# Optimization experiments

Measured on AMD Instinct MI355X. Metric: run time of the kernel, lower is better.

## Reference

```python
import jax, jax.numpy as jnp
import numpy as np

B, D_IMG, D_TXT, E = 4096, 768, 768, 512
LAMBDA_CMP = 1.0
EPS = 1e-10


def setup_inputs() -> dict:
    key = jax.random.key(0)
    k1, k2, k3, k4, k5 = jax.random.split(key, 5)
    return {
        "images": jax.random.normal(k1, (B, D_IMG), dtype=jnp.float32),
        "texts": jax.random.normal(k2, (B, D_TXT), dtype=jnp.float32),
        "labels": jax.random.randint(k3, (B,), 0, 1000, dtype=jnp.int32),
        "W_img": jax.random.normal(k4, (D_IMG, E), dtype=jnp.float32) / np.sqrt(D_IMG),
        "W_txt": jax.random.normal(k5, (D_TXT, E), dtype=jnp.float32) / np.sqrt(D_TXT),
        "logit_scale": jnp.asarray(np.log(1.0 / 0.07), dtype=jnp.float32),
    }


def reference(images, texts, labels, W_img, W_txt, logit_scale):
    # CLIP-style encoders: linear project + L2 normalize
    img = images @ W_img
    txt = texts @ W_txt
    img = img / jnp.linalg.norm(img, axis=-1, keepdims=True)
    txt = txt / jnp.linalg.norm(txt, axis=-1, keepdims=True)
    logits = jnp.exp(logit_scale) * (img @ txt.T)  # [B, B]

    b = logits.shape[0]
    rows = jnp.arange(b)
    logp = jax.nn.log_softmax(logits, axis=-1)
    clip_loss = -jnp.mean(logp[rows, labels])

    probs = jnp.exp(logp)                # softmax probs [B, B]
    p_yi = probs[rows, labels]           # [B]
    # columns j whose label differs from sample i's label AND prob exceeds p_yi
    diff_label = labels[None, :] != labels[:, None]           # [B, B]
    mask = diff_label & (probs > p_yi[:, None])               # [B, B]
    denom = jnp.sum(jnp.where(mask, probs, 0.0), axis=1)      # [B]
    has_any = jnp.any(mask, axis=1)
    cmp_loss = jnp.sum(jnp.where(has_any, p_yi / (denom + EPS), 0.0)) / b

    return clip_loss + LAMBDA_CMP * cmp_loss
```

## Files before the change

### kernel.cpp

```cpp
#include <hip/hip_runtime.h>
#include <stdint.h>

#define BATCH 4096
#define DDIM  768
#define EDIM  512
#define NSPLIT 16
#define LOG2E 1.44269504088896340736f

using short8  = __attribute__((ext_vector_type(8))) short;
using float4v = __attribute__((ext_vector_type(4))) float;

__device__ __forceinline__ unsigned short f2bf(float x) {
    union { float f; uint32_t u; } v; v.f = x;
    uint32_t u = v.u;
    u += 0x7FFFu + ((u >> 16) & 1u);
    return (unsigned short)(u >> 16);
}
__device__ __forceinline__ float bf2f(unsigned short h) {
    union { uint32_t u; float f; } v; v.u = ((uint32_t)h) << 16;
    return v.f;
}

__device__ __forceinline__ short8 cvt8(float4 v0, float4 v1) {
    union { short8 s8; uint32_t w[4]; } u;
    asm("v_cvt_pk_bf16_f32 %0, %1, %2" : "=v"(u.w[0]) : "v"(v0.x), "v"(v0.y));
    asm("v_cvt_pk_bf16_f32 %0, %1, %2" : "=v"(u.w[1]) : "v"(v0.z), "v"(v0.w));
    asm("v_cvt_pk_bf16_f32 %0, %1, %2" : "=v"(u.w[2]) : "v"(v1.x), "v"(v1.y));
    asm("v_cvt_pk_bf16_f32 %0, %1, %2" : "=v"(u.w[3]) : "v"(v1.z), "v"(v1.w));
    return u.s8;
}

__device__ __forceinline__ void gl2lds16(const void* g, void* l) {
    __builtin_amdgcn_global_load_lds(
        (const __attribute__((address_space(1))) void*)g,
        (__attribute__((address_space(3))) void*)l, 16, 0, 0);
}

__global__ void transpose2(const float* __restrict__ Wa, const float* __restrict__ Wb,
                           unsigned short* __restrict__ Ta, unsigned short* __restrict__ Tb) {
    const float* W = blockIdx.z ? Wb : Wa;
    unsigned short* Wt = blockIdx.z ? Tb : Ta;
    __shared__ float tile[32][33];
    int n0 = blockIdx.x * 32, k0 = blockIdx.y * 32;
    int tid = threadIdx.x;
    for (int p = 0; p < 4; ++p) {
        int e = tid + p * 256; int lr = e >> 5, lc = e & 31;
        tile[lc][lr] = W[(size_t)(k0 + lr) * EDIM + n0 + lc];
    }
    __syncthreads();
    for (int p = 0; p < 4; ++p) {
        int e = tid + p * 256; int lr = e >> 5, lc = e & 31;
        Wt[(size_t)(n0 + lr) * DDIM + k0 + lc] = f2bf(tile[lr][lc]);
    }
}

__global__ __launch_bounds__(256) void gemm_nt(const float* __restrict__ Aimg,
                                               const float* __restrict__ Atxt,
                                               const unsigned short* __restrict__ Bimg,
                                               const unsigned short* __restrict__ Btxt,
                                               unsigned short* __restrict__ Cimg,
                                               unsigned short* __restrict__ Ctxt) {
    const float* A           = blockIdx.z ? Atxt : Aimg;
    const unsigned short* Bm = blockIdx.z ? Btxt : Bimg;
    unsigned short* C        = blockIdx.z ? Ctxt : Cimg;
    __shared__ __align__(16) float As[2][128 * 64];
    __shared__ __align__(16) unsigned short Bs[2][64 * 64];
    int tid = threadIdx.x;
    int wave = tid >> 6, lane = tid & 63;
    int q = lane >> 4, r = lane & 15;
    int m0 = blockIdx.x * 128, n0 = blockIdx.y * 64;
    int sw = (r >> 1) & 3;

    const float* gsA[8];
    float* lsA[8];
    for (int i = 0; i < 8; ++i) {
        int p = i * 256 + tid;
        int row = p >> 4, kqp = p & 15;
        int kq = kqp ^ (row & 7);
        gsA[i] = &A[(size_t)(m0 + row) * DDIM + kq * 4];
        lsA[i] = &As[0][p * 4];
    }
    const unsigned short* gsB[2];
    unsigned short* lsB[2];
    for (int i = 0; i < 2; ++i) {
        int u = i * 256 + tid;
        int kc2 = u >> 8, row = (u >> 2) & 63, kq = u & 3;
        int kq2 = kq ^ ((row >> 1) & 3);
        gsB[i] = &Bm[(size_t)(n0 + row) * DDIM + kc2 * 32 + kq2 * 8];
        lsB[i] = &Bs[0][u * 8];
    }

    float4v acc[2][4];
    for (int a = 0; a < 2; ++a)
        for (int t = 0; t < 4; ++t) acc[a][t] = (float4v){0.f, 0.f, 0.f, 0.f};

    for (int i = 0; i < 8; ++i) gl2lds16(gsA[i], lsA[i]);
    for (int i = 0; i < 2; ++i) gl2lds16(gsB[i], lsB[i]);
    __syncthreads();

    for (int it = 0; it < DDIM / 64; ++it) {
        int b = it & 1;
        if (it < DDIM / 64 - 1) {
            int k0 = (it + 1) * 64;
            for (int i = 0; i < 8; ++i) gl2lds16(gsA[i] + k0, lsA[i] + (b ^ 1) * (128 * 64));
            for (int i = 0; i < 2; ++i) gl2lds16(gsB[i] + k0, lsB[i] + (b ^ 1) * (64 * 64));
        }
        #pragma unroll
        for (int kc2 = 0; kc2 < 2; ++kc2) {
            int R0r = wave * 32 + r;
            int g0 = kc2 * 8 + (q ^ sw) * 2;
            int e = R0r & 7;
            int p0 = g0 ^ e, p1 = (g0 + 1) ^ e;
            float4 v0 = *(const float4*)&As[b][R0r * 64 + p0 * 4];
            float4 v1 = *(const float4*)&As[b][R0r * 64 + p1 * 4];
            float4 w0 = *(const float4*)&As[b][(R0r + 16) * 64 + p0 * 4];
            float4 w1 = *(const float4*)&As[b][(R0r + 16) * 64 + p1 * 4];
            short8 a0 = cvt8(v0, v1);
            short8 a1 = cvt8(w0, w1);
            #pragma unroll
            for (int t = 0; t < 4; ++t) {
                short8 bfr = *(const short8*)&Bs[b][kc2 * 2048 + (t * 16 + r) * 32 + (q ^ sw) * 8];
                acc[0][t] = __builtin_amdgcn_mfma_f32_16x16x32_bf16(a0, bfr, acc[0][t], 0, 0, 0);
                acc[1][t] = __builtin_amdgcn_mfma_f32_16x16x32_bf16(a1, bfr, acc[1][t], 0, 0, 0);
            }
        }
        __syncthreads();
    }
    for (int rg = 0; rg < 2; ++rg)
        for (int t = 0; t < 4; ++t)
            for (int g = 0; g < 4; ++g)
                C[(size_t)(m0 + wave * 32 + rg * 16 + q * 4 + g) * EDIM + n0 + t * 16 + r] =
                    f2bf(acc[rg][t][g]);
}

__global__ void rnorm(const unsigned short* __restrict__ pi, const unsigned short* __restrict__ pt,
                      const int* __restrict__ labels,
                      float* __restrict__ rn_i, float* __restrict__ rn_t,
                      float* __restrict__ tout) {
    int wave = threadIdx.x >> 6, lane = threadIdx.x & 63;
    int row = blockIdx.x * 4 + wave;
    int lab = labels[row];
    union { unsigned short us[8]; uint4 u4; } a, b, c;
    a.u4 = *(const uint4*)&pi[(size_t)row * 512 + lane * 8];
    b.u4 = *(const uint4*)&pt[(size_t)row * 512 + lane * 8];
    c.u4 = *(const uint4*)&pt[(size_t)lab * 512 + lane * 8];
    float si = 0.f, st = 0.f, sl = 0.f, dt = 0.f;
    #pragma unroll
    for (int j = 0; j < 8; ++j) {
        float fa = bf2f(a.us[j]), fb = bf2f(b.us[j]), fc = bf2f(c.us[j]);
        si += fa * fa; st += fb * fb; sl += fc * fc; dt += fa * fc;
    }
    for (int off = 1; off < 64; off <<= 1) {
        si += __shfl_xor(si, off);
        st += __shfl_xor(st, off);
        sl += __shfl_xor(sl, off);
        dt += __shfl_xor(dt, off);
    }
    if (lane == 0) {
        float ri = rsqrtf(si);
        rn_i[row] = ri;
        rn_t[row] = rsqrtf(st);
        tout[row] = dt * ri * rsqrtf(sl);
    }
}

__global__ __launch_bounds__(256) void flash_pass(
    const unsigned short* __restrict__ img, const unsigned short* __restrict__ txt,
    const int* __restrict__ labels, const float* __restrict__ tvals,
    const float* __restrict__ rn_i, const float* __restrict__ rn_t,
    const float* __restrict__ ls,
    float* __restrict__ lP, float* __restrict__ dP) {
    __shared__ __align__(16) unsigned short Bs[8 * 64 * 32];
    int tid = threadIdx.x;
    int wave = tid >> 6, lane = tid & 63;
    int q = lane >> 4, r = lane & 15;
    int row0 = blockIdx.x * 64 + wave * 16;
    int split = blockIdx.y;
    float alpha = expf(ls[0]);
    float c1 = alpha * LOG2E;

    int srow = tid >> 2, skp = tid & 3;
    int skp2 = skp ^ ((srow >> 1) & 3);
    int sw = (r >> 1) & 3;

    short8 af[16];
    for (int kc = 0; kc < 16; ++kc)
        af[kc] = *(const short8*)&img[(size_t)(row0 + r) * 512 + kc * 32 + q * 8];

    int labr[4]; float tr[4], rnr[4];
    for (int g = 0; g < 4; ++g) {
        int rw = row0 + q * 4 + g;
        labr[g] = labels[rw];
        tr[g] = tvals[rw];
        rnr[g] = rn_i[rw];
    }
    float l[4] = {0.f, 0.f, 0.f, 0.f}, d[4] = {0.f, 0.f, 0.f, 0.f};

    for (int ct = 0; ct < 4; ++ct) {
        int colbase = split * 256 + ct * 64;
        const unsigned short* gB = &txt[(size_t)(colbase + srow) * 512 + skp2 * 8];
        float4v acc[4];
        for (int t = 0; t < 4; ++t) acc[t] = (float4v){0.f, 0.f, 0.f, 0.f};
        for (int h = 0; h < 2; ++h) {
            __syncthreads();
            for (int i = 0; i < 8; ++i)
                gl2lds16(gB + h * 256 + i * 32, &Bs[i * 2048 + tid * 8]);
            __syncthreads();
            for (int kc = 0; kc < 8; ++kc) {
                short8 a = af[h * 8 + kc];
                for (int t = 0; t < 4; ++t) {
                    short8 bf = *(const short8*)&Bs[(kc * 64 + t * 16 + r) * 32 + (q ^ sw) * 8];
                    acc[t] = __builtin_amdgcn_mfma_f32_16x16x32_bf16(a, bf, acc[t], 0, 0, 0);
                }
            }
        }
        for (int t = 0; t < 4; ++t) {
            int cix = colbase + t * 16 + r;
            int lc = labels[cix];
            float rc = rn_t[cix];
            for (int g = 0; g < 4; ++g) {
                float a = acc[t][g] * (rc * rnr[g]);
                float p = exp2f(fmaf(a, c1, -c1));
                l[g] += p;
                d[g] += ((a > tr[g]) && (lc != labr[g])) ? p : 0.f;
            }
        }
    }
    for (int g = 0; g < 4; ++g) {
        float lv = l[g], dv = d[g];
        for (int off = 1; off < 16; off <<= 1) {
            lv += __shfl_xor(lv, off);
            dv += __shfl_xor(dv, off);
        }
        if (r == 0) {
            int rw = row0 + q * 4 + g;
            lP[(size_t)rw * NSPLIT + split] = lv;
            dP[(size_t)rw * NSPLIT + split] = dv;
        }
    }
}

__global__ void combine(const float* __restrict__ lP, const float* __restrict__ dP,
                        const float* __restrict__ tvals, const float* __restrict__ ls,
                        float* __restrict__ out) {
    int row = blockIdx.x * 256 + threadIdx.x;
    float alpha = expf(ls[0]);
    float L = 0.f, D = 0.f;
    for (int s = 0; s < NSPLIT; ++s) {
        L += lP[(size_t)row * NSPLIT + s];
        D += dP[(size_t)row * NSPLIT + s];
    }
    float tm = alpha * (tvals[row] - 1.0f);
    float clip = logf(L) - tm;
    float py = expf(tm) / L;
    float cmp = (D > 0.f) ? py / (D / L + 1e-10f) : 0.f;
    float v = clip + cmp;
    for (int off = 1; off < 64; off <<= 1) v += __shfl_xor(v, off);
    __shared__ float w4[4];
    int wave = threadIdx.x >> 6, lane = threadIdx.x & 63;
    if (lane == 0) w4[wave] = v;
    __syncthreads();
    if (threadIdx.x == 0)
        atomicAdd(out, (w4[0] + w4[1] + w4[2] + w4[3]) * (1.0f / BATCH));
}

extern "C" void kernel_launch(void* const* d_in, const int* in_sizes, int n_in,
                              void* d_out, int out_size, void* d_ws, size_t ws_size,
                              hipStream_t stream) {
    const float* images = (const float*)d_in[0];
    const float* texts  = (const float*)d_in[1];
    const int*   labels = (const int*)d_in[2];
    const float* W_img  = (const float*)d_in[3];
    const float* W_txt  = (const float*)d_in[4];
    const float* lscale = (const float*)d_in[5];
    float* out = (float*)d_out;

    char* ws = (char*)d_ws;
    unsigned short* wt_img = (unsigned short*)(ws + 0);
    unsigned short* wt_txt = (unsigned short*)(ws + 786432);
    unsigned short* proj_i = (unsigned short*)(ws + 1572864);
    unsigned short* proj_t = (unsigned short*)(ws + 5767168);
    float*          rn_img = (float*)(ws + 9961472);
    float*          rn_txt = (float*)(ws + 9977856);
    float*          tvals  = (float*)(ws + 9994240);
    float*          lP     = (float*)(ws + 10010624);
    float*          dP     = (float*)(ws + 10272768);

    hipMemsetAsync(out, 0, sizeof(float), stream);
    transpose2<<<dim3(EDIM / 32, DDIM / 32, 2), 256, 0, stream>>>(W_img, W_txt, wt_img, wt_txt);
    gemm_nt<<<dim3(BATCH / 128, EDIM / 64, 2), 256, 0, stream>>>(images, texts, wt_img, wt_txt,
                                                                 proj_i, proj_t);
    rnorm<<<BATCH / 4, 256, 0, stream>>>(proj_i, proj_t, labels, rn_img, rn_txt, tvals);
    flash_pass<<<dim3(BATCH / 64, NSPLIT), 256, 0, stream>>>(proj_i, proj_t, labels, tvals,
                                                             rn_img, rn_txt, lscale, lP, dP);
    combine<<<16, 256, 0, stream>>>(lP, dP, tvals, lscale, out);
}
```

Before: 134.6 us.

## Double-buffer text tiles in flash pass with smaller column chunks and swapped grid

Restructures the flash_pass inner loop to double-buffer the text B tiles in LDS. Each step prefetches the next 32-column by 256-K chunk while MFMAs consume the current one, which removes one of the two barriers per stage. The column tile shrinks from 64 to 32, halving accumulators, and the loops are fully unrolled. The grid is transposed so that consecutive blocks share the same text split, improving L2 reuse. The trade-off is more loop iterations, fewer MFMAs per barrier, and higher register pressure from the unrolling.

```diff
diff --git a/kernel.cpp b/kernel.cpp
--- a/kernel.cpp
+++ b/kernel.cpp
@@ -170,18 +170,29 @@
     const float* __restrict__ rn_i, const float* __restrict__ rn_t,
     const float* __restrict__ ls,
     float* __restrict__ lP, float* __restrict__ dP) {
-    __shared__ __align__(16) unsigned short Bs[8 * 64 * 32];
+    __shared__ __align__(16) unsigned short Bs[2][8192];
     int tid = threadIdx.x;
     int wave = tid >> 6, lane = tid & 63;
     int q = lane >> 4, r = lane & 15;
-    int row0 = blockIdx.x * 64 + wave * 16;
-    int split = blockIdx.y;
+    int split = blockIdx.x;
+    int row0 = blockIdx.y * 64 + wave * 16;
     float alpha = expf(ls[0]);
     float c1 = alpha * LOG2E;
 
-    int srow = tid >> 2, skp = tid & 3;
-    int skp2 = skp ^ ((srow >> 1) & 3);
+    int scol = (tid >> 2) & 31, skp = tid & 3;
+    int skp2 = skp ^ ((scol >> 1) & 3);
     int sw = (r >> 1) & 3;
+
+    const unsigned short* gsB[4];
+    int lsB[4];
+    for (int i = 0; i < 4; ++i) {
+        int u = i * 256 + tid;
+        int kc = u >> 7;
+        gsB[i] = &txt[(size_t)(split * 256 + scol) * 512 + kc * 32 + skp2 * 8];
+        lsB[i] = u * 8;
+    }
+
+    for (int i = 0; i < 4; ++i) gl2lds16(gsB[i], &Bs[0][lsB[i]]);
 
     short8 af[16];
     for (int kc = 0; kc < 16; ++kc)
@@ -195,35 +206,52 @@
         rnr[g] = rn_i[rw];
     }
     float l[4] = {0.f, 0.f, 0.f, 0.f}, d[4] = {0.f, 0.f, 0.f, 0.f};
-
-    for (int ct = 0; ct < 4; ++ct) {
-        int colbase = split * 256 + ct * 64;
-        const unsigned short* gB = &txt[(size_t)(colbase + srow) * 512 + skp2 * 8];
-        float4v acc[4];
-        for (int t = 0; t < 4; ++t) acc[t] = (float4v){0.f, 0.f, 0.f, 0.f};
+    float4v acc[2];
+    acc[0] = (float4v){0.f, 0.f, 0.f, 0.f};
+    acc[1] = (float4v){0.f, 0.f, 0.f, 0.f};
+
+    __syncthreads();
+
+    #pragma unroll
+    for (int ct2 = 0; ct2 < 8; ++ct2) {
+        #pragma unroll
         for (int h = 0; h < 2; ++h) {
-            __syncthreads();
-            for (int i = 0; i < 8; ++i)
-                gl2lds16(gB + h * 256 + i * 32, &Bs[i * 2048 + tid * 8]);
-            __syncthreads();
+            int s = ct2 * 2 + h;
+            int buf = s & 1;
+            if (s < 15) {
+                int sn = s + 1;
+                int goff = (sn >> 1) * (32 * 512) + (sn & 1) * 256;
+                #pragma unroll
+                for (int i = 0; i < 4; ++i)
+                    gl2lds16(gsB[i] + goff, &Bs[buf ^ 1][lsB[i]]);
+            }
+            #pragma unroll
             for (int kc = 0; kc < 8; ++kc) {
                 short8 a = af[h * 8 + kc];
-                for (int t = 0; t < 4; ++t) {
-                    short8 bf = *(const short8*)&Bs[(kc * 64 + t * 16 + r) * 32 + (q ^ sw) * 8];
+                #pragma unroll
+                for (int t = 0; t < 2; ++t) {
+                    short8 bf = *(const short8*)&Bs[buf][kc * 1024 + (t * 16 + r) * 32 + (q ^ sw) * 8];
                     acc[t] = __builtin_amdgcn_mfma_f32_16x16x32_bf16(a, bf, acc[t], 0, 0, 0);
                 }
             }
-        }
-        for (int t = 0; t < 4; ++t) {
-            int cix = colbase + t * 16 + r;
-            int lc = labels[cix];
-            float rc = rn_t[cix];
-            for (int g = 0; g < 4; ++g) {
-                float a = acc[t][g] * (rc * rnr[g]);
-                float p = exp2f(fmaf(a, c1, -c1));
-                l[g] += p;
-                d[g] += ((a > tr[g]) && (lc != labr[g])) ? p : 0.f;
+            if (h == 1) {
+                int colbase = split * 256 + ct2 * 32;
+                #pragma unroll
+                for (int t = 0; t < 2; ++t) {
+                    int cix = colbase + t * 16 + r;
+                    int lc = labels[cix];
+                    float rc = rn_t[cix];
+                    #pragma unroll
+                    for (int g = 0; g < 4; ++g) {
+                        float a = acc[t][g] * (rc * rnr[g]);
+                        float p = exp2f(fmaf(a, c1, -c1));
+                        l[g] += p;
+                        d[g] += ((a > tr[g]) && (lc != labr[g])) ? p : 0.f;
+                    }
+                    acc[t] = (float4v){0.f, 0.f, 0.f, 0.f};
+                }
             }
+            __syncthreads();
         }
     }
     for (int g = 0; g < 4; ++g) {
@@ -291,7 +319,7 @@
     gemm_nt<<<dim3(BATCH / 128, EDIM / 64, 2), 256, 0, stream>>>(images, texts, wt_img, wt_txt,
                                                                  proj_i, proj_t);
     rnorm<<<BATCH / 4, 256, 0, stream>>>(proj_i, proj_t, labels, rn_img, rn_txt, tvals);
-    flash_pass<<<dim3(BATCH / 64, NSPLIT), 256, 0, stream>>>(proj_i, proj_t, labels, tvals,
+    flash_pass<<<dim3(NSPLIT, BATCH / 64), 256, 0, stream>>>(proj_i, proj_t, labels, tvals,
                                                              rn_img, rn_txt, lscale, lP, dP);
     combine<<<16, 256, 0, stream>>>(lP, dP, tvals, lscale, out);
 }
```

New measurement: 133.7 us. No clear change (-0.7%).
